# Kernel tuning notes

Measured on AMD Instinct MI355X. Metric: run time of the kernel, lower is better.

The kernel has to match this reference:

```python
import jax, jax.numpy as jnp
import numpy as np

N_NODES, N_EDGES, N_FEAT, DIM, HEADS, N_PRED, N_CLASS, N_STEPS = 10000, 160000, 64, 64, 4, 2, 16, 4


def setup_inputs() -> dict:
    key = jax.random.key(0)
    ks = jax.random.split(key, 16)
    def lin(k, fi, fo):
        return jax.random.normal(k, (fi, fo), jnp.float32) / np.sqrt(fi)
    return {
        "x": jax.random.normal(ks[0], (N_NODES, N_FEAT), jnp.float32),
        "edge_index": jax.random.randint(ks[1], (2, N_EDGES), 0, N_NODES, jnp.int64),
        "enc_W": lin(ks[2], N_FEAT, DIM), "enc_b": jnp.zeros((DIM,), jnp.float32),
        "gat_Wl": lin(ks[3], DIM, HEADS * DIM), "gat_bl": jnp.zeros((HEADS * DIM,), jnp.float32),
        "gat_Wr": lin(ks[4], DIM, HEADS * DIM), "gat_br": jnp.zeros((HEADS * DIM,), jnp.float32),
        "gat_att": jax.random.normal(ks[5], (HEADS, DIM), jnp.float32) / np.sqrt(DIM),
        "gat_bias": jnp.zeros((HEADS * DIM,), jnp.float32),
        "W1": lin(ks[6], HEADS * DIM, DIM), "b1": jnp.zeros((DIM,), jnp.float32),
        "W2": lin(ks[7], DIM, DIM), "b2": jnp.zeros((DIM,), jnp.float32),
        "act_W": lin(ks[8], DIM, 1), "act_b": jnp.zeros((1,), jnp.float32),
        "dec_W": jax.random.normal(ks[9], (N_PRED, DIM, N_CLASS), jnp.float32) / np.sqrt(DIM),
        "dec_b": jnp.zeros((N_PRED, N_CLASS), jnp.float32),
        "num_steps": N_STEPS,
    }


def reference(x, edge_index, enc_W, enc_b, gat_Wl, gat_bl, gat_Wr, gat_br,
              gat_att, gat_bias, W1, b1, W2, b2, act_W, act_b, dec_W, dec_b, num_steps):
    N = x.shape[0]
    H, C = gat_att.shape  # heads, per-head channels
    # PyG GATv2Conv adds self-loops by default
    loops = jnp.arange(N, dtype=edge_index.dtype)
    src = jnp.concatenate([edge_index[0], loops])
    dst = jnp.concatenate([edge_index[1], loops])

    h0 = x @ enc_W + enc_b  # encoder

    def step(carry, _):
        h, total, final = carry
        # GATv2: per-edge score on lin_l(src) + lin_r(dst)
        xl = (h @ gat_Wl + gat_bl).reshape(N, H, C)
        xr = (h @ gat_Wr + gat_br).reshape(N, H, C)
        e = jax.nn.leaky_relu(xl[src] + xr[dst], 0.2)          # [E, H, C]
        logits = jnp.einsum('ehc,hc->eh', e, gat_att)           # [E, H]
        m = jax.ops.segment_max(logits, dst, num_segments=N)    # segment softmax over dst
        ex = jnp.exp(logits - m[dst])
        denom = jax.ops.segment_sum(ex, dst, num_segments=N)
        alpha = ex / (denom[dst] + 1e-16)
        agg = jax.ops.segment_sum(xl[src] * alpha[:, :, None], dst, num_segments=N)
        g = agg.reshape(N, H * C) + gat_bias                    # concat heads + bias
        hn = jax.nn.relu(g @ W1 + b1) @ W2 + b2                 # process2 MLP
        # ACT halting: weighted accumulation, deltas clipped so weights sum to <= 1
        term = jax.nn.sigmoid(hn @ act_W + act_b)               # [N, 1]
        new_total = jnp.minimum(total + term, 1.0)
        delta = jnp.minimum(term, new_total - total)
        return (hn, total + delta, final + delta * hn), None

    carry0 = (h0, jnp.zeros((N, 1), x.dtype), jnp.zeros((N, h0.shape[1]), x.dtype))
    (_, _, final), _ = jax.lax.scan(step, carry0, None, length=num_steps)

    logits = jnp.einsum('nd,pdc->pnc', final, dec_W) + dec_b[:, None, :]
    return jax.nn.log_softmax(logits, axis=-1)  # [num_predictions, N, num_classes]
```

## Files before the change

### kernel.cpp

```cpp
#include <hip/hip_runtime.h>
#include <hip/hip_bf16.h>
#include <hip/hip_fp16.h>

#define N_NODES 10000
#define N_EDGES 160000
#define N_E2    (N_EDGES + N_NODES)
#define DIM     64
#define HD      256
#define N_PRED  2
#define N_CLASS 16
#define N_STEPS 4

typedef __hip_bfloat16 bf16;
__device__ __forceinline__ float b2f(bf16 v) { return __bfloat162float(v); }
__device__ __forceinline__ int clampn(int v) { return v < 0 ? 0 : (v >= N_NODES ? N_NODES - 1 : v); }

typedef _Float16 h2_t __attribute__((ext_vector_type(2)));

__device__ __forceinline__ float dot2(unsigned int a, unsigned int b, float c) {
#if __has_builtin(__builtin_amdgcn_fdot2)
    h2_t av, bv;
    __builtin_memcpy(&av, &a, 4);
    __builtin_memcpy(&bv, &b, 4);
    return __builtin_amdgcn_fdot2(av, bv, c, false);
#else
    __half2 ah = *(__half2*)&a, bh = *(__half2*)&b;
    float2 af = __half22float2(ah), bf = __half22float2(bh);
    return c + af.x * bf.x + af.y * bf.y;
#endif
}

struct ConvTable {
    const void* src[17];
    int start[18];
};

__global__ void detect_kernel(const unsigned int* __restrict__ e32,
                              const unsigned short* __restrict__ x16,
                              int* __restrict__ flags) {
    __shared__ int ce, cf;
    if (threadIdx.x == 0) { ce = 0; cf = 0; }
    __syncthreads();
    int le = 0;
    for (int i = threadIdx.x; i < 2048; i += 256)
        le += (e32[2 * i + 1] != 0u) ? 1 : 0;
    int lf = 0;
    for (int i = threadIdx.x; i < 1024; i += 256) {
        unsigned short u = x16[2 * i];
        int ex = (u >> 7) & 0xFF;
        lf += (u == 0 || (ex >= 114 && ex <= 141)) ? 1 : 0;
    }
    atomicAdd(&ce, le);
    atomicAdd(&cf, lf);
    __syncthreads();
    if (threadIdx.x == 0) {
        flags[0] = (ce < 1024) ? 1 : 0;
        flags[1] = (cf >= 512) ? 1 : 0;
    }
}

__global__ void convert_kernel(ConvTable tab, const int* __restrict__ flags,
                               float* __restrict__ xf) {
    int i = blockIdx.x * 256 + threadIdx.x;
    if (i >= tab.start[17]) return;
    int j = 0;
    #pragma unroll
    for (int k = 1; k < 17; ++k) j += (i >= tab.start[k]) ? 1 : 0;
    int off = i - tab.start[j];
    float v;
    if (flags[1]) v = b2f(((const bf16*)tab.src[j])[off]);
    else          v = ((const float*)tab.src[j])[off];
    xf[i] = v;
}

__global__ void pack_kernel(const float* __restrict__ xf,
                            int oWl, int oWr, int oW1, int oW2,
                            __half* __restrict__ wp) {
    int i = blockIdx.x * 256 + threadIdx.x;
    if (i >= 26624) return;
    int base, width, loc;
    if (i < 8192)       { loc = i;         base = oWl; width = 256; }
    else if (i < 16384) { loc = i - 8192;  base = oWr; width = 256; }
    else if (i < 24576) { loc = i - 16384; base = oW1; width = 64; }
    else                { loc = i - 24576; base = oW2; width = 64; }
    int k2 = loc / width, c = loc % width;
    wp[2 * i]     = __float2half(xf[base + (2 * k2) * width + c]);
    wp[2 * i + 1] = __float2half(xf[base + (2 * k2 + 1) * width + c]);
}

__global__ void hist_kernel(const int* __restrict__ edges, const int* __restrict__ flags,
                            int* __restrict__ deg) {
    int e = blockIdx.x * 256 + threadIdx.x;
    if (e >= N_E2) return;
    int i64 = flags[0];
    int dst;
    if (e < N_EDGES) dst = clampn(i64 ? edges[2 * (N_EDGES + e)] : edges[N_EDGES + e]);
    else             dst = e - N_EDGES;
    atomicAdd(&deg[dst], 1);
}

__global__ void scan_kernel(const int* __restrict__ deg, int* __restrict__ off) {
    __shared__ int partial[1024];
    const int tid = threadIdx.x;
    const int per = (N_NODES + 1023) / 1024;
    int local[16];
    int base = tid * per;
    int s = 0;
    for (int i = 0; i < per; ++i) {
        int v = (base + i < N_NODES) ? deg[base + i] : 0;
        local[i] = s;
        s += v;
    }
    partial[tid] = s;
    __syncthreads();
    for (int d = 1; d < 1024; d <<= 1) {
        int t = (tid >= d) ? partial[tid - d] : 0;
        __syncthreads();
        partial[tid] += t;
        __syncthreads();
    }
    int offset = (tid > 0) ? partial[tid - 1] : 0;
    for (int i = 0; i < per; ++i)
        if (base + i < N_NODES) off[base + i] = offset + local[i];
    if (tid == 1023) off[N_NODES] = partial[1023];
}

__global__ void scatter_kernel(const int* __restrict__ edges, const int* __restrict__ flags,
                               const int* __restrict__ off, int* __restrict__ cursor,
                               int* __restrict__ csr_src) {
    int e = blockIdx.x * 256 + threadIdx.x;
    if (e >= N_E2) return;
    int i64 = flags[0];
    int src, dst;
    if (e < N_EDGES) {
        src = clampn(i64 ? edges[2 * e] : edges[e]);
        dst = clampn(i64 ? edges[2 * (N_EDGES + e)] : edges[N_EDGES + e]);
    } else { src = dst = e - N_EDGES; }
    int pos = off[dst] + atomicAdd(&cursor[dst], 1);
    csr_src[pos] = src;
}

__global__ __launch_bounds__(256) void enc_proj_kernel(
        const float* __restrict__ Xf,
        const float* __restrict__ encW, const float* __restrict__ encB,
        const float* __restrict__ Wl, const float* __restrict__ bl,
        const float* __restrict__ Wr, const float* __restrict__ br,
        __half* __restrict__ xlh, float* __restrict__ xr) {
    __shared__ float xs[8][DIM];
    __shared__ float h0[8][DIM];
    const int t = threadIdx.x, pp = t >> 6, d = t & 63;
    const int n0 = blockIdx.x * 8;
    ((float*)xs)[t]       = Xf[n0 * DIM + t];
    ((float*)xs)[t + 256] = Xf[n0 * DIM + t + 256];
    __syncthreads();
    float ah0 = encB[d], ah1 = encB[d];
    for (int k = 0; k < DIM; ++k) {
        float wv = encW[k * DIM + d];
        ah0 += xs[pp][k] * wv;
        ah1 += xs[pp + 4][k] * wv;
    }
    h0[pp][d]     = ah0;
    h0[pp + 4][d] = ah1;
    __syncthreads();
    float al[8] = {0,0,0,0,0,0,0,0}, ar[8] = {0,0,0,0,0,0,0,0};
    for (int k = 0; k < DIM; ++k) {
        float wl = Wl[k * HD + t], wr = Wr[k * HD + t];
        #pragma unroll
        for (int j = 0; j < 8; ++j) { al[j] += h0[j][k] * wl; ar[j] += h0[j][k] * wr; }
    }
    float bbl = bl[t], bbr = br[t];
    #pragma unroll
    for (int j = 0; j < 8; ++j) {
        xlh[(size_t)(n0 + j) * HD + t] = __float2half(al[j] + bbl);
        xr[(size_t)(n0 + j) * HD + t] = ar[j] + bbr;
    }
}

__global__ __launch_bounds__(256) void edge_agg_kernel(
        const __half* __restrict__ xlh, const float* __restrict__ xr,
        const float* __restrict__ att, const float* __restrict__ gbias,
        const int* __restrict__ off, const int* __restrict__ csr_src,
        __half* __restrict__ gbufh) {
    const int t = threadIdx.x, w = t >> 6, l = t & 63;
    const int n = blockIdx.x * 4 + w;
    const int e0 = off[n], e1 = off[n + 1];
    const int elast = e1 - 1;
    const float4 xr4 = ((const float4*)(xr + (size_t)n * HD))[l];
    const float4 at4 = ((const float4*)att)[l];

    float m = -1e30f, s = 0.f;
    float4 acc = {0.f, 0.f, 0.f, 0.f};
    uint2 A[4], B[4];
    #pragma unroll
    for (int i = 0; i < 4; ++i) {
        int ee = e0 + i; ee = (ee > elast) ? elast : ee;
        A[i] = ((const uint2*)(xlh + (size_t)csr_src[ee] * HD))[l];
    }
    for (int base = e0; base < e1; base += 4) {
        #pragma unroll
        for (int i = 0; i < 4; ++i) {
            int ee = base + 4 + i; ee = (ee > elast) ? elast : ee;
            B[i] = ((const uint2*)(xlh + (size_t)csr_src[ee] * HD))[l];
        }
        #pragma unroll
        for (int i = 0; i < 4; ++i) {
            const bool valid = (base + i) < e1;
            __half2 h01 = *reinterpret_cast<__half2*>(&A[i].x);
            __half2 h23 = *reinterpret_cast<__half2*>(&A[i].y);
            float2 f01 = __half22float2(h01);
            float2 f23 = __half22float2(h23);
            float c0 = f01.x, c1 = f01.y, c2 = f23.x, c3 = f23.y;
            float z0 = c0 + xr4.x, z1 = c1 + xr4.y, z2 = c2 + xr4.z, z3 = c3 + xr4.w;
            z0 = (z0 > 0.f) ? z0 : 0.2f * z0;
            z1 = (z1 > 0.f) ? z1 : 0.2f * z1;
            z2 = (z2 > 0.f) ? z2 : 0.2f * z2;
            z3 = (z3 > 0.f) ? z3 : 0.2f * z3;
            float p = z0 * at4.x + z1 * at4.y + z2 * at4.z + z3 * at4.w;
            #pragma unroll
            for (int mo = 8; mo; mo >>= 1) p += __shfl_xor(p, mo, 64);
            p = valid ? p : -1e30f;
            float nm = fmaxf(m, p);
            float sc = __expf(m - nm);
            float wv = __expf(p - nm);
            s = s * sc + wv;
            acc.x = acc.x * sc + wv * c0;
            acc.y = acc.y * sc + wv * c1;
            acc.z = acc.z * sc + wv * c2;
            acc.w = acc.w * sc + wv * c3;
            m = nm;
        }
        #pragma unroll
        for (int i = 0; i < 4; ++i) A[i] = B[i];
    }
    const float inv = 1.f / (s + 1e-16f);
    const float4 gb4 = ((const float4*)gbias)[l];
    __half2 o01 = __floats2half2_rn(acc.x * inv + gb4.x, acc.y * inv + gb4.y);
    __half2 o23 = __floats2half2_rn(acc.z * inv + gb4.z, acc.w * inv + gb4.w);
    uint2 outv;
    outv.x = *(unsigned int*)&o01;
    outv.y = *(unsigned int*)&o23;
    ((uint2*)(gbufh + (size_t)n * HD))[l] = outv;
}

__global__ __launch_bounds__(256) void mlp_act_proj_kernel(
        const __half* __restrict__ gbufh, const __half* __restrict__ wp,
        const float* __restrict__ b1, const float* __restrict__ b2,
        const float* __restrict__ actW, const float* __restrict__ actB,
        const float* __restrict__ bl, const float* __restrict__ br,
        float* __restrict__ act_tot, float* __restrict__ final_,
        __half* __restrict__ xlh, float* __restrict__ xr, int do_proj) {
    __shared__ unsigned int gall_u[4][128];
    __shared__ float part[4][HD];
    __shared__ __half us_h[4][DIM];
    __shared__ float hns[4][DIM];
    __shared__ __half hns_h[4][DIM];
    __shared__ float delta[4];
    const int t = threadIdx.x, pp = t >> 6, d = t & 63;
    const int n0 = blockIdx.x * 4;

    const unsigned int* Wlp = (const unsigned int*)wp;
    const unsigned int* Wrp = Wlp + 8192;
    const unsigned int* W1p = Wlp + 16384;
    const unsigned int* W2p = Wlp + 24576;

    {
        const unsigned int* gb = (const unsigned int*)gbufh;
        ((unsigned int*)gall_u)[t]       = gb[(size_t)n0 * 128 + t];
        ((unsigned int*)gall_u)[t + 256] = gb[(size_t)n0 * 128 + t + 256];
    }
    __syncthreads();

    {
        float acc[4] = {0.f, 0.f, 0.f, 0.f};
        for (int k2 = pp * 32; k2 < pp * 32 + 32; ++k2) {
            unsigned int w2 = W1p[k2 * 64 + d];
            #pragma unroll
            for (int j = 0; j < 4; ++j) acc[j] = dot2(gall_u[j][k2], w2, acc[j]);
        }
        #pragma unroll
        for (int j = 0; j < 4; ++j) part[j][t] = acc[j];
    }
    __syncthreads();
    {
        float v = part[pp][d] + part[pp][64 + d] + part[pp][128 + d] + part[pp][192 + d] + b1[d];
        us_h[pp][d] = __float2half(fmaxf(v, 0.f));
    }
    __syncthreads();

    {
        const unsigned int* us_u = (const unsigned int*)us_h;
        float acc[4] = {0.f, 0.f, 0.f, 0.f};
        for (int k2 = pp * 8; k2 < pp * 8 + 8; ++k2) {
            unsigned int w2 = W2p[k2 * 64 + d];
            #pragma unroll
            for (int j = 0; j < 4; ++j) acc[j] = dot2(us_u[j * 32 + k2], w2, acc[j]);
        }
        #pragma unroll
        for (int j = 0; j < 4; ++j) part[j][t] = acc[j];
    }
    __syncthreads();
    {
        float hv = part[pp][d] + part[pp][64 + d] + part[pp][128 + d] + part[pp][192 + d] + b2[d];
        hns[pp][d] = hv;
        hns_h[pp][d] = __float2half(hv);
    }
    __syncthreads();

    {
        float p = hns[pp][d] * actW[d];
        #pragma unroll
        for (int mo = 32; mo; mo >>= 1) p += __shfl_xor(p, mo, 64);
        if (d == 0) {
            float term = 1.f / (1.f + __expf(-(p + actB[0])));
            float tot = act_tot[n0 + pp];
            float nt = fminf(tot + term, 1.f);
            float dl = fminf(term, nt - tot);
            act_tot[n0 + pp] = tot + dl;
            delta[pp] = dl;
        }
    }
    __syncthreads();
    final_[(size_t)(n0 + pp) * DIM + d] += delta[pp] * hns[pp][d];

    if (do_proj) {
        const unsigned int* hn_u = (const unsigned int*)hns_h;
        float al[4] = {0.f, 0.f, 0.f, 0.f}, ar[4] = {0.f, 0.f, 0.f, 0.f};
        for (int k2 = 0; k2 < 32; ++k2) {
            unsigned int wl2 = Wlp[k2 * 256 + t];
            unsigned int wr2 = Wrp[k2 * 256 + t];
            #pragma unroll
            for (int j = 0; j < 4; ++j) {
                unsigned int hh = hn_u[j * 32 + k2];
                al[j] = dot2(hh, wl2, al[j]);
                ar[j] = dot2(hh, wr2, ar[j]);
            }
        }
        float bbl = bl[t], bbr = br[t];
        #pragma unroll
        for (int j = 0; j < 4; ++j) {
            xlh[(size_t)(n0 + j) * HD + t] = __float2half(al[j] + bbl);
            xr[(size_t)(n0 + j) * HD + t] = ar[j] + bbr;
        }
    }
}

__global__ void decoder_kernel(const float* __restrict__ final_,
                               const float* __restrict__ decW, const float* __restrict__ decB,
                               const int* __restrict__ flags, void* __restrict__ outv) {
    int id = blockIdx.x * 256 + threadIdx.x;
    if (id >= N_NODES * N_PRED * N_CLASS) return;
    int n = id >> 5, r = id & 31, p = r >> 4, c = r & 15;
    float acc = decB[p * N_CLASS + c];
    for (int dd = 0; dd < DIM; ++dd)
        acc += final_[(size_t)n * DIM + dd] * decW[(p * DIM + dd) * N_CLASS + c];
    float mx = acc;
    #pragma unroll
    for (int mo = 8; mo; mo >>= 1) mx = fmaxf(mx, __shfl_xor(mx, mo, 64));
    float ex = __expf(acc - mx);
    float ss = ex;
    #pragma unroll
    for (int mo = 8; mo; mo >>= 1) ss += __shfl_xor(ss, mo, 64);
    float ov = acc - mx - logf(ss);
    int oi = p * (N_NODES * N_CLASS) + n * N_CLASS + c;
    if (flags[1]) ((bf16*)outv)[oi] = __float2bfloat16(ov);
    else          ((float*)outv)[oi] = ov;
}

static size_t align256(size_t x) { return (x + 255) & ~size_t(255); }

extern "C" void kernel_launch(void* const* d_in, const int* in_sizes, int n_in,
                              void* d_out, int out_size, void* d_ws, size_t ws_size,
                              hipStream_t stream) {
    const int* edges = (const int*)d_in[1];

    static const int fids[17] = {0, 2, 3, 4, 5, 6, 7, 8, 9, 10, 11, 12, 13, 14, 15, 16, 17};
    ConvTable tab;
    int cum = 0;
    for (int i = 0; i < 17; ++i) {
        tab.src[i] = d_in[fids[i]];
        tab.start[i] = cum;
        cum += in_sizes[fids[i]];
    }
    tab.start[17] = cum;

    char* w = (char*)d_ws;
    size_t o = 0;
    int* flags     = (int*)(w + o); o = align256(o + 16 * sizeof(int));
    int* off       = (int*)(w + o); o = align256(o + (N_NODES + 1) * sizeof(int));
    size_t zbase = o;
    int* deg       = (int*)(w + o); o = align256(o + N_NODES * sizeof(int));
    int* cursor    = (int*)(w + o); o = align256(o + N_NODES * sizeof(int));
    float* act_tot = (float*)(w + o); o = align256(o + N_NODES * sizeof(float));
    float* final_  = (float*)(w + o); o = align256(o + (size_t)N_NODES * DIM * sizeof(float));
    size_t zsize = o - zbase;
    int* csr_src   = (int*)(w + o); o = align256(o + N_E2 * sizeof(int));
    float* xf      = (float*)(w + o); o = align256(o + (size_t)cum * sizeof(float));
    __half* xlh    = (__half*)(w + o); o = align256(o + (size_t)N_NODES * HD * sizeof(__half));
    float* xr      = (float*)(w + o); o = align256(o + (size_t)N_NODES * HD * sizeof(float));
    __half* gbufh  = (__half*)(w + o); o = align256(o + (size_t)N_NODES * HD * sizeof(__half));
    __half* wpack  = (__half*)(w + o); o = align256(o + 53248 * sizeof(__half));
    if (o > ws_size) return;

    const float* Xf   = xf + tab.start[0];
    const float* encW = xf + tab.start[1];
    const float* encB = xf + tab.start[2];
    const float* Wl   = xf + tab.start[3];
    const float* bl   = xf + tab.start[4];
    const float* Wr   = xf + tab.start[5];
    const float* br   = xf + tab.start[6];
    const float* att  = xf + tab.start[7];
    const float* gbias= xf + tab.start[8];
    const float* b1   = xf + tab.start[10];
    const float* b2   = xf + tab.start[12];
    const float* actW = xf + tab.start[13];
    const float* actB = xf + tab.start[14];
    const float* decW = xf + tab.start[15];
    const float* decB = xf + tab.start[16];

    hipMemsetAsync(w + zbase, 0, zsize, stream);

    detect_kernel<<<1, 256, 0, stream>>>((const unsigned int*)d_in[1],
                                         (const unsigned short*)d_in[0], flags);
    convert_kernel<<<(cum + 255) / 256, 256, 0, stream>>>(tab, flags, xf);
    pack_kernel<<<(26624 + 255) / 256, 256, 0, stream>>>(
        xf, tab.start[3], tab.start[5], tab.start[9], tab.start[11], wpack);

    int eb = (N_E2 + 255) / 256;
    hist_kernel<<<eb, 256, 0, stream>>>(edges, flags, deg);
    scan_kernel<<<1, 1024, 0, stream>>>(deg, off);
    scatter_kernel<<<eb, 256, 0, stream>>>(edges, flags, off, cursor, csr_src);

    enc_proj_kernel<<<N_NODES / 8, 256, 0, stream>>>(Xf, encW, encB, Wl, bl, Wr, br, xlh, xr);

    for (int step = 0; step < N_STEPS; ++step) {
        edge_agg_kernel<<<N_NODES / 4, 256, 0, stream>>>(xlh, xr, att, gbias, off, csr_src, gbufh);
        mlp_act_proj_kernel<<<N_NODES / 4, 256, 0, stream>>>(
            gbufh, wpack, b1, b2, actW, actB, bl, br,
            act_tot, final_, xlh, xr, (step < N_STEPS - 1) ? 1 : 0);
    }

    int db = (N_NODES * N_PRED * N_CLASS + 255) / 256;
    decoder_kernel<<<db, 256, 0, stream>>>(final_, decW, decB, flags, d_out);
}
```

Baseline: 324.4 us.

## Fuse edge aggregation into MLP step kernel and merge setup kernels

Merges the per-step edge-aggregation and MLP/projection kernels into one step kernel. The aggregated features stay in shared memory instead of round-tripping through a global buffer, and xl/xr are ping-ponged between two buffers to avoid read/write hazards. Setup work (convert, pack, histogram) is merged into one launch, as is scatter plus encoder. The memset is replaced by zeroing inside existing kernels. This cuts launch count and global traffic, at the cost of higher shared/register pressure in the fused step kernel.

```diff
diff --git a/kernel.cpp b/kernel.cpp
--- a/kernel.cpp
+++ b/kernel.cpp
@@ -35,9 +35,14 @@
     int start[18];
 };
 
+__device__ __forceinline__ float loadf(const void* p, int idx, int isbf16) {
+    return isbf16 ? b2f(((const bf16*)p)[idx]) : ((const float*)p)[idx];
+}
+
 __global__ void detect_kernel(const unsigned int* __restrict__ e32,
                               const unsigned short* __restrict__ x16,
-                              int* __restrict__ flags) {
+                              int* __restrict__ flags,
+                              int* __restrict__ deg, int* __restrict__ cursor) {
     __shared__ int ce, cf;
     if (threadIdx.x == 0) { ce = 0; cf = 0; }
     __syncthreads();
@@ -52,6 +57,7 @@
     }
     atomicAdd(&ce, le);
     atomicAdd(&cf, lf);
+    for (int i = threadIdx.x; i < N_NODES; i += 256) { deg[i] = 0; cursor[i] = 0; }
     __syncthreads();
     if (threadIdx.x == 0) {
         flags[0] = (ce < 1024) ? 1 : 0;
@@ -59,44 +65,45 @@
     }
 }
 
-__global__ void convert_kernel(ConvTable tab, const int* __restrict__ flags,
-                               float* __restrict__ xf) {
-    int i = blockIdx.x * 256 + threadIdx.x;
-    if (i >= tab.start[17]) return;
-    int j = 0;
-    #pragma unroll
-    for (int k = 1; k < 17; ++k) j += (i >= tab.start[k]) ? 1 : 0;
-    int off = i - tab.start[j];
-    float v;
-    if (flags[1]) v = b2f(((const bf16*)tab.src[j])[off]);
-    else          v = ((const float*)tab.src[j])[off];
-    xf[i] = v;
-}
-
-__global__ void pack_kernel(const float* __restrict__ xf,
-                            int oWl, int oWr, int oW1, int oW2,
-                            __half* __restrict__ wp) {
-    int i = blockIdx.x * 256 + threadIdx.x;
-    if (i >= 26624) return;
-    int base, width, loc;
-    if (i < 8192)       { loc = i;         base = oWl; width = 256; }
-    else if (i < 16384) { loc = i - 8192;  base = oWr; width = 256; }
-    else if (i < 24576) { loc = i - 16384; base = oW1; width = 64; }
-    else                { loc = i - 24576; base = oW2; width = 64; }
-    int k2 = loc / width, c = loc % width;
-    wp[2 * i]     = __float2half(xf[base + (2 * k2) * width + c]);
-    wp[2 * i + 1] = __float2half(xf[base + (2 * k2 + 1) * width + c]);
-}
-
-__global__ void hist_kernel(const int* __restrict__ edges, const int* __restrict__ flags,
-                            int* __restrict__ deg) {
-    int e = blockIdx.x * 256 + threadIdx.x;
-    if (e >= N_E2) return;
-    int i64 = flags[0];
-    int dst;
-    if (e < N_EDGES) dst = clampn(i64 ? edges[2 * (N_EDGES + e)] : edges[N_EDGES + e]);
-    else             dst = e - N_EDGES;
-    atomicAdd(&deg[dst], 1);
+struct PreArgs {
+    ConvTable tab;
+    const void* Wl_raw; const void* Wr_raw; const void* W1_raw; const void* W2_raw;
+    const int* edges;
+    int cb, pb;
+};
+
+__global__ void pre_kernel(PreArgs a, const int* __restrict__ flags,
+                           float* __restrict__ xf, __half* __restrict__ wp,
+                           int* __restrict__ deg) {
+    const int b = blockIdx.x, t = threadIdx.x;
+    const int isb = flags[1];
+    if (b < a.cb) {
+        int i = b * 256 + t;
+        if (i >= a.tab.start[17]) return;
+        int j = 0;
+        #pragma unroll
+        for (int k = 1; k < 17; ++k) j += (i >= a.tab.start[k]) ? 1 : 0;
+        xf[i] = loadf(a.tab.src[j], i - a.tab.start[j], isb);
+    } else if (b < a.cb + a.pb) {
+        int i = (b - a.cb) * 256 + t;
+        if (i >= 26624) return;
+        const void* base; int width, loc;
+        if (i < 8192)       { loc = i;         base = a.Wl_raw; width = 256; }
+        else if (i < 16384) { loc = i - 8192;  base = a.Wr_raw; width = 256; }
+        else if (i < 24576) { loc = i - 16384; base = a.W1_raw; width = 64; }
+        else                { loc = i - 24576; base = a.W2_raw; width = 64; }
+        int k2 = loc / width, c = loc % width;
+        wp[2 * i]     = __float2half(loadf(base, (2 * k2) * width + c, isb));
+        wp[2 * i + 1] = __float2half(loadf(base, (2 * k2 + 1) * width + c, isb));
+    } else {
+        int e = (b - a.cb - a.pb) * 256 + t;
+        if (e >= N_E2) return;
+        int i64 = flags[0];
+        int dst;
+        if (e < N_EDGES) dst = clampn(i64 ? a.edges[2 * (N_EDGES + e)] : a.edges[N_EDGES + e]);
+        else             dst = e - N_EDGES;
+        atomicAdd(&deg[dst], 1);
+    }
 }
 
 __global__ void scan_kernel(const int* __restrict__ deg, int* __restrict__ off) {
@@ -125,33 +132,51 @@
     if (tid == 1023) off[N_NODES] = partial[1023];
 }
 
-__global__ void scatter_kernel(const int* __restrict__ edges, const int* __restrict__ flags,
-                               const int* __restrict__ off, int* __restrict__ cursor,
-                               int* __restrict__ csr_src) {
-    int e = blockIdx.x * 256 + threadIdx.x;
-    if (e >= N_E2) return;
-    int i64 = flags[0];
-    int src, dst;
-    if (e < N_EDGES) {
-        src = clampn(i64 ? edges[2 * e] : edges[e]);
-        dst = clampn(i64 ? edges[2 * (N_EDGES + e)] : edges[N_EDGES + e]);
-    } else { src = dst = e - N_EDGES; }
-    int pos = off[dst] + atomicAdd(&cursor[dst], 1);
-    csr_src[pos] = src;
-}
-
-__global__ __launch_bounds__(256) void enc_proj_kernel(
-        const float* __restrict__ Xf,
-        const float* __restrict__ encW, const float* __restrict__ encB,
-        const float* __restrict__ Wl, const float* __restrict__ bl,
-        const float* __restrict__ Wr, const float* __restrict__ br,
-        __half* __restrict__ xlh, float* __restrict__ xr) {
+struct SEArgs {
+    const int* edges;
+    const int* off;
+    int* cursor;
+    int* csr_src;
+    const float* xf;
+    int sX, sEncW, sEncB, sWl, sBl, sWr, sBr;
+    __half* xlh;
+    float* xr;
+    float* act_tot;
+    float* final_;
+    int sb;
+};
+
+__global__ __launch_bounds__(256) void scatter_enc_kernel(SEArgs a, const int* __restrict__ flags) {
+    const int b = blockIdx.x, t = threadIdx.x;
+    if (b < a.sb) {
+        int e = b * 256 + t;
+        if (e >= N_E2) return;
+        int i64 = flags[0];
+        int src, dst;
+        if (e < N_EDGES) {
+            src = clampn(i64 ? a.edges[2 * e] : a.edges[e]);
+            dst = clampn(i64 ? a.edges[2 * (N_EDGES + e)] : a.edges[N_EDGES + e]);
+        } else { src = dst = e - N_EDGES; }
+        int pos = a.off[dst] + atomicAdd(&a.cursor[dst], 1);
+        a.csr_src[pos] = src;
+        return;
+    }
     __shared__ float xs[8][DIM];
     __shared__ float h0[8][DIM];
-    const int t = threadIdx.x, pp = t >> 6, d = t & 63;
-    const int n0 = blockIdx.x * 8;
+    const int pp = t >> 6, d = t & 63;
+    const int n0 = (b - a.sb) * 8;
+    const float* Xf   = a.xf + a.sX;
+    const float* encW = a.xf + a.sEncW;
+    const float* encB = a.xf + a.sEncB;
+    const float* Wl   = a.xf + a.sWl;
+    const float* bl   = a.xf + a.sBl;
+    const float* Wr   = a.xf + a.sWr;
+    const float* br   = a.xf + a.sBr;
     ((float*)xs)[t]       = Xf[n0 * DIM + t];
     ((float*)xs)[t + 256] = Xf[n0 * DIM + t + 256];
+    a.final_[(size_t)n0 * DIM + t]       = 0.f;
+    a.final_[(size_t)n0 * DIM + t + 256] = 0.f;
+    if (t < 8) a.act_tot[n0 + t] = 0.f;
     __syncthreads();
     float ah0 = encB[d], ah1 = encB[d];
     for (int k = 0; k < DIM; ++k) {
@@ -171,92 +196,91 @@
     float bbl = bl[t], bbr = br[t];
     #pragma unroll
     for (int j = 0; j < 8; ++j) {
-        xlh[(size_t)(n0 + j) * HD + t] = __float2half(al[j] + bbl);
-        xr[(size_t)(n0 + j) * HD + t] = ar[j] + bbr;
-    }
-}
-
-__global__ __launch_bounds__(256) void edge_agg_kernel(
-        const __half* __restrict__ xlh, const float* __restrict__ xr,
+        a.xlh[(size_t)(n0 + j) * HD + t] = __float2half(al[j] + bbl);
+        a.xr[(size_t)(n0 + j) * HD + t] = ar[j] + bbr;
+    }
+}
+
+__global__ __launch_bounds__(256) void step_kernel(
+        const __half* __restrict__ xlh_in, const float* __restrict__ xr_in,
         const float* __restrict__ att, const float* __restrict__ gbias,
         const int* __restrict__ off, const int* __restrict__ csr_src,
-        __half* __restrict__ gbufh) {
-    const int t = threadIdx.x, w = t >> 6, l = t & 63;
-    const int n = blockIdx.x * 4 + w;
-    const int e0 = off[n], e1 = off[n + 1];
-    const int elast = e1 - 1;
-    const float4 xr4 = ((const float4*)(xr + (size_t)n * HD))[l];
-    const float4 at4 = ((const float4*)att)[l];
-
-    float m = -1e30f, s = 0.f;
-    float4 acc = {0.f, 0.f, 0.f, 0.f};
-    uint2 A[4], B[4];
-    #pragma unroll
-    for (int i = 0; i < 4; ++i) {
-        int ee = e0 + i; ee = (ee > elast) ? elast : ee;
-        A[i] = ((const uint2*)(xlh + (size_t)csr_src[ee] * HD))[l];
-    }
-    for (int base = e0; base < e1; base += 4) {
-        #pragma unroll
-        for (int i = 0; i < 4; ++i) {
-            int ee = base + 4 + i; ee = (ee > elast) ? elast : ee;
-            B[i] = ((const uint2*)(xlh + (size_t)csr_src[ee] * HD))[l];
-        }
-        #pragma unroll
-        for (int i = 0; i < 4; ++i) {
-            const bool valid = (base + i) < e1;
-            __half2 h01 = *reinterpret_cast<__half2*>(&A[i].x);
-            __half2 h23 = *reinterpret_cast<__half2*>(&A[i].y);
-            float2 f01 = __half22float2(h01);
-            float2 f23 = __half22float2(h23);
-            float c0 = f01.x, c1 = f01.y, c2 = f23.x, c3 = f23.y;
-            float z0 = c0 + xr4.x, z1 = c1 + xr4.y, z2 = c2 + xr4.z, z3 = c3 + xr4.w;
-            z0 = (z0 > 0.f) ? z0 : 0.2f * z0;
-            z1 = (z1 > 0.f) ? z1 : 0.2f * z1;
-            z2 = (z2 > 0.f) ? z2 : 0.2f * z2;
-            z3 = (z3 > 0.f) ? z3 : 0.2f * z3;
-            float p = z0 * at4.x + z1 * at4.y + z2 * at4.z + z3 * at4.w;
-            #pragma unroll
-            for (int mo = 8; mo; mo >>= 1) p += __shfl_xor(p, mo, 64);
-            p = valid ? p : -1e30f;
-            float nm = fmaxf(m, p);
-            float sc = __expf(m - nm);
-            float wv = __expf(p - nm);
-            s = s * sc + wv;
-            acc.x = acc.x * sc + wv * c0;
-            acc.y = acc.y * sc + wv * c1;
-            acc.z = acc.z * sc + wv * c2;
-            acc.w = acc.w * sc + wv * c3;
-            m = nm;
-        }
-        #pragma unroll
-        for (int i = 0; i < 4; ++i) A[i] = B[i];
-    }
-    const float inv = 1.f / (s + 1e-16f);
-    const float4 gb4 = ((const float4*)gbias)[l];
-    __half2 o01 = __floats2half2_rn(acc.x * inv + gb4.x, acc.y * inv + gb4.y);
-    __half2 o23 = __floats2half2_rn(acc.z * inv + gb4.z, acc.w * inv + gb4.w);
-    uint2 outv;
-    outv.x = *(unsigned int*)&o01;
-    outv.y = *(unsigned int*)&o23;
-    ((uint2*)(gbufh + (size_t)n * HD))[l] = outv;
-}
-
-__global__ __launch_bounds__(256) void mlp_act_proj_kernel(
-        const __half* __restrict__ gbufh, const __half* __restrict__ wp,
+        const __half* __restrict__ wp,
         const float* __restrict__ b1, const float* __restrict__ b2,
         const float* __restrict__ actW, const float* __restrict__ actB,
         const float* __restrict__ bl, const float* __restrict__ br,
         float* __restrict__ act_tot, float* __restrict__ final_,
-        __half* __restrict__ xlh, float* __restrict__ xr, int do_proj) {
-    __shared__ unsigned int gall_u[4][128];
+        __half* __restrict__ xlh_out, float* __restrict__ xr_out, int do_proj) {
+    __shared__ __align__(16) unsigned int gall_u[4][128];
     __shared__ float part[4][HD];
     __shared__ __half us_h[4][DIM];
     __shared__ float hns[4][DIM];
     __shared__ __half hns_h[4][DIM];
     __shared__ float delta[4];
-    const int t = threadIdx.x, pp = t >> 6, d = t & 63;
+    const int t = threadIdx.x, w = t >> 6, l = t & 63;
+    const int pp = w, d = l;
     const int n0 = blockIdx.x * 4;
+    const int n = n0 + w;
+
+    {
+        const int e0 = off[n], e1 = off[n + 1];
+        const int elast = e1 - 1;
+        const float4 xr4 = ((const float4*)(xr_in + (size_t)n * HD))[l];
+        const float4 at4 = ((const float4*)att)[l];
+        float m = -1e30f, s = 0.f;
+        float4 acc = {0.f, 0.f, 0.f, 0.f};
+        uint2 A[4], B[4];
+        #pragma unroll
+        for (int i = 0; i < 4; ++i) {
+            int ee = e0 + i; ee = (ee > elast) ? elast : ee;
+            A[i] = ((const uint2*)(xlh_in + (size_t)csr_src[ee] * HD))[l];
+        }
+        for (int base = e0; base < e1; base += 4) {
+            #pragma unroll
+            for (int i = 0; i < 4; ++i) {
+                int ee = base + 4 + i; ee = (ee > elast) ? elast : ee;
+                B[i] = ((const uint2*)(xlh_in + (size_t)csr_src[ee] * HD))[l];
+            }
+            #pragma unroll
+            for (int i = 0; i < 4; ++i) {
+                const bool valid = (base + i) < e1;
+                __half2 h01 = *reinterpret_cast<__half2*>(&A[i].x);
+                __half2 h23 = *reinterpret_cast<__half2*>(&A[i].y);
+                float2 f01 = __half22float2(h01);
+                float2 f23 = __half22float2(h23);
+                float c0 = f01.x, c1 = f01.y, c2 = f23.x, c3 = f23.y;
+                float z0 = c0 + xr4.x, z1 = c1 + xr4.y, z2 = c2 + xr4.z, z3 = c3 + xr4.w;
+                z0 = (z0 > 0.f) ? z0 : 0.2f * z0;
+                z1 = (z1 > 0.f) ? z1 : 0.2f * z1;
+                z2 = (z2 > 0.f) ? z2 : 0.2f * z2;
+                z3 = (z3 > 0.f) ? z3 : 0.2f * z3;
+                float p = z0 * at4.x + z1 * at4.y + z2 * at4.z + z3 * at4.w;
+                #pragma unroll
+                for (int mo = 8; mo; mo >>= 1) p += __shfl_xor(p, mo, 64);
+                p = valid ? p : -1e30f;
+                float nm = fmaxf(m, p);
+                float sc = __expf(m - nm);
+                float wv = __expf(p - nm);
+                s = s * sc + wv;
+                acc.x = acc.x * sc + wv * c0;
+                acc.y = acc.y * sc + wv * c1;
+                acc.z = acc.z * sc + wv * c2;
+                acc.w = acc.w * sc + wv * c3;
+                m = nm;
+            }
+            #pragma unroll
+            for (int i = 0; i < 4; ++i) A[i] = B[i];
+        }
+        const float inv = 1.f / (s + 1e-16f);
+        const float4 gb4 = ((const float4*)gbias)[l];
+        __half2 o01 = __floats2half2_rn(acc.x * inv + gb4.x, acc.y * inv + gb4.y);
+        __half2 o23 = __floats2half2_rn(acc.z * inv + gb4.z, acc.w * inv + gb4.w);
+        uint2 outv;
+        outv.x = *(unsigned int*)&o01;
+        outv.y = *(unsigned int*)&o23;
+        ((uint2*)gall_u[w])[l] = outv;
+    }
+    __syncthreads();
 
     const unsigned int* Wlp = (const unsigned int*)wp;
     const unsigned int* Wrp = Wlp + 8192;
@@ -264,13 +288,6 @@
     const unsigned int* W2p = Wlp + 24576;
 
     {
-        const unsigned int* gb = (const unsigned int*)gbufh;
-        ((unsigned int*)gall_u)[t]       = gb[(size_t)n0 * 128 + t];
-        ((unsigned int*)gall_u)[t + 256] = gb[(size_t)n0 * 128 + t + 256];
-    }
-    __syncthreads();
-
-    {
         float acc[4] = {0.f, 0.f, 0.f, 0.f};
         for (int k2 = pp * 32; k2 < pp * 32 + 32; ++k2) {
             unsigned int w2 = W1p[k2 * 64 + d];
@@ -286,7 +303,6 @@
         us_h[pp][d] = __float2half(fmaxf(v, 0.f));
     }
     __syncthreads();
-
     {
         const unsigned int* us_u = (const unsigned int*)us_h;
         float acc[4] = {0.f, 0.f, 0.f, 0.f};
@@ -305,7 +321,6 @@
         hns_h[pp][d] = __float2half(hv);
     }
     __syncthreads();
-
     {
         float p = hns[pp][d] * actW[d];
         #pragma unroll
@@ -338,8 +353,8 @@
         float bbl = bl[t], bbr = br[t];
         #pragma unroll
         for (int j = 0; j < 4; ++j) {
-            xlh[(size_t)(n0 + j) * HD + t] = __float2half(al[j] + bbl);
-            xr[(size_t)(n0 + j) * HD + t] = ar[j] + bbr;
+            xlh_out[(size_t)(n0 + j) * HD + t] = __float2half(al[j] + bbl);
+            xr_out[(size_t)(n0 + j) * HD + t] = ar[j] + bbr;
         }
     }
 }
@@ -387,27 +402,19 @@
     size_t o = 0;
     int* flags     = (int*)(w + o); o = align256(o + 16 * sizeof(int));
     int* off       = (int*)(w + o); o = align256(o + (N_NODES + 1) * sizeof(int));
-    size_t zbase = o;
     int* deg       = (int*)(w + o); o = align256(o + N_NODES * sizeof(int));
     int* cursor    = (int*)(w + o); o = align256(o + N_NODES * sizeof(int));
     float* act_tot = (float*)(w + o); o = align256(o + N_NODES * sizeof(float));
     float* final_  = (float*)(w + o); o = align256(o + (size_t)N_NODES * DIM * sizeof(float));
-    size_t zsize = o - zbase;
     int* csr_src   = (int*)(w + o); o = align256(o + N_E2 * sizeof(int));
     float* xf      = (float*)(w + o); o = align256(o + (size_t)cum * sizeof(float));
-    __half* xlh    = (__half*)(w + o); o = align256(o + (size_t)N_NODES * HD * sizeof(__half));
-    float* xr      = (float*)(w + o); o = align256(o + (size_t)N_NODES * HD * sizeof(float));
-    __half* gbufh  = (__half*)(w + o); o = align256(o + (size_t)N_NODES * HD * sizeof(__half));
+    __half* xlh_a  = (__half*)(w + o); o = align256(o + (size_t)N_NODES * HD * sizeof(__half));
+    float* xr_a    = (float*)(w + o); o = align256(o + (size_t)N_NODES * HD * sizeof(float));
+    __half* xlh_b  = (__half*)(w + o); o = align256(o + (size_t)N_NODES * HD * sizeof(__half));
+    float* xr_b    = (float*)(w + o); o = align256(o + (size_t)N_NODES * HD * sizeof(float));
     __half* wpack  = (__half*)(w + o); o = align256(o + 53248 * sizeof(__half));
     if (o > ws_size) return;
 
-    const float* Xf   = xf + tab.start[0];
-    const float* encW = xf + tab.start[1];
-    const float* encB = xf + tab.start[2];
-    const float* Wl   = xf + tab.start[3];
-    const float* bl   = xf + tab.start[4];
-    const float* Wr   = xf + tab.start[5];
-    const float* br   = xf + tab.start[6];
     const float* att  = xf + tab.start[7];
     const float* gbias= xf + tab.start[8];
     const float* b1   = xf + tab.start[10];
@@ -417,26 +424,39 @@
     const float* decW = xf + tab.start[15];
     const float* decB = xf + tab.start[16];
 
-    hipMemsetAsync(w + zbase, 0, zsize, stream);
-
     detect_kernel<<<1, 256, 0, stream>>>((const unsigned int*)d_in[1],
-                                         (const unsigned short*)d_in[0], flags);
-    convert_kernel<<<(cum + 255) / 256, 256, 0, stream>>>(tab, flags, xf);
-    pack_kernel<<<(26624 + 255) / 256, 256, 0, stream>>>(
-        xf, tab.start[3], tab.start[5], tab.start[9], tab.start[11], wpack);
-
-    int eb = (N_E2 + 255) / 256;
-    hist_kernel<<<eb, 256, 0, stream>>>(edges, flags, deg);
+                                         (const unsigned short*)d_in[0], flags, deg, cursor);
+
+    PreArgs pa;
+    pa.tab = tab;
+    pa.Wl_raw = d_in[4]; pa.Wr_raw = d_in[6]; pa.W1_raw = d_in[10]; pa.W2_raw = d_in[12];
+    pa.edges = edges;
+    pa.cb = (cum + 255) / 256;
+    pa.pb = (26624 + 255) / 256;
+    int hb = (N_E2 + 255) / 256;
+    pre_kernel<<<pa.cb + pa.pb + hb, 256, 0, stream>>>(pa, flags, xf, wpack, deg);
+
     scan_kernel<<<1, 1024, 0, stream>>>(deg, off);
-    scatter_kernel<<<eb, 256, 0, stream>>>(edges, flags, off, cursor, csr_src);
-
-    enc_proj_kernel<<<N_NODES / 8, 256, 0, stream>>>(Xf, encW, encB, Wl, bl, Wr, br, xlh, xr);
-
+
+    SEArgs se;
+    se.edges = edges; se.off = off; se.cursor = cursor; se.csr_src = csr_src;
+    se.xf = xf;
+    se.sX = tab.start[0]; se.sEncW = tab.start[1]; se.sEncB = tab.start[2];
+    se.sWl = tab.start[3]; se.sBl = tab.start[4]; se.sWr = tab.start[5]; se.sBr = tab.start[6];
+    se.xlh = xlh_a; se.xr = xr_a; se.act_tot = act_tot; se.final_ = final_;
+    se.sb = hb;
+    scatter_enc_kernel<<<hb + N_NODES / 8, 256, 0, stream>>>(se, flags);
+
+    __half* xl_in = xlh_a;  float* xr_in = xr_a;
+    __half* xl_out = xlh_b; float* xr_out = xr_b;
     for (int step = 0; step < N_STEPS; ++step) {
-        edge_agg_kernel<<<N_NODES / 4, 256, 0, stream>>>(xlh, xr, att, gbias, off, csr_src, gbufh);
-        mlp_act_proj_kernel<<<N_NODES / 4, 256, 0, stream>>>(
-            gbufh, wpack, b1, b2, actW, actB, bl, br,
-            act_tot, final_, xlh, xr, (step < N_STEPS - 1) ? 1 : 0);
+        step_kernel<<<N_NODES / 4, 256, 0, stream>>>(
+            xl_in, xr_in, att, gbias, off, csr_src, wpack,
+            b1, b2, actW, actB,
+            xf + tab.start[4], xf + tab.start[6],
+            act_tot, final_, xl_out, xr_out, (step < N_STEPS - 1) ? 1 : 0);
+        __half* th = xl_in; xl_in = xl_out; xl_out = th;
+        float* tf = xr_in; xr_in = xr_out; xr_out = tf;
     }
 
     int db = (N_NODES * N_PRED * N_CLASS + 255) / 256;
```

Result: faster. 298.6 us (-8.0%).
